# Kernel optimization log

Hardware: AMD Instinct MI355X
Metric: run time of the kernel (lower is better)

## Reference

```python
import jax, jax.numpy as jnp
import numpy as np

B, N, D_POINTS, D_MODEL = 8, 2048, 64, 512


def _linear_params(key, d_in, d_out, bias=True):
    k1, k2 = jax.random.split(key)
    bound = 1.0 / np.sqrt(d_in)
    W = jax.random.uniform(k1, (d_in, d_out), jnp.float32, -bound, bound)
    if not bias:
        return W
    b = jax.random.uniform(k2, (d_out,), jnp.float32, -bound, bound)
    return W, b


def setup_inputs() -> dict:
    key = jax.random.key(0)
    ks = jax.random.split(key, 10)
    xyz = jax.random.normal(ks[0], (B, N, 3), jnp.float32)
    features = jax.random.normal(ks[1], (B, N, D_POINTS), jnp.float32)
    W1, b1 = _linear_params(ks[2], D_POINTS, D_MODEL)      # fc1
    W2, b2 = _linear_params(ks[3], D_MODEL, D_POINTS)      # fc2
    Wd1, bd1 = _linear_params(ks[4], 3, D_MODEL)           # fc_delta[0]
    Wd2, bd2 = _linear_params(ks[5], D_MODEL, D_MODEL)     # fc_delta[2]
    Wq = _linear_params(ks[6], D_MODEL, D_MODEL, bias=False)
    Wk = _linear_params(ks[7], D_MODEL, D_MODEL, bias=False)
    Wv = _linear_params(ks[8], D_MODEL, D_MODEL, bias=False)
    return {"xyz": xyz, "features": features,
            "W1": W1, "b1": b1, "W2": W2, "b2": b2,
            "Wd1": Wd1, "bd1": bd1, "Wd2": Wd2, "bd2": bd2,
            "Wq": Wq, "Wk": Wk, "Wv": Wv, "k": 16}


def _forward(xyz, features, W1, b1, W2, b2, Wd1, bd1, Wd2, bd2, Wq, Wk, Wv, k):
    # square_distance: ||xi - xj||^2, [B, N, N]
    sq = jnp.sum(xyz * xyz, axis=-1)
    dists = sq[:, :, None] + sq[:, None, :] - 2.0 * jnp.einsum('bnd,bmd->bnm', xyz, xyz)
    knn_idx = jnp.argsort(dists, axis=-1)[:, :, :k]              # [B, N, k]
    knn_xyz = jax.vmap(lambda p, i: p[i])(xyz, knn_idx)          # [B, N, k, 3]

    pre = features
    x = features @ W1 + b1                                       # [B, N, d_model]
    q, key, v = x @ Wq, x @ Wk, x @ Wv

    # fc_delta on gathered neighbor coordinates -> [B, N, k, d_model]
    pos_enc = jax.nn.relu(knn_xyz @ Wd1 + bd1) @ Wd2 + bd2

    eps = 1e-06
    knn_d = jnp.take_along_axis(dists, knn_idx, axis=2)          # [B, N, k]
    weights = 1.0 / (knn_d + eps)
    weighted_avg = jnp.sum(pos_enc * weights[..., None], axis=2) / \
        jnp.sum(weights, axis=2, keepdims=True)                  # [B, N, d_model]

    scale = 1.0 / np.sqrt(D_MODEL)
    score = jnp.einsum('bnd,bmd->bnm', q + weighted_avg, key + weighted_avg) * scale
    attn_map = jax.nn.softmax(score, axis=-1)                    # [B, N, N]
    attn = jnp.einsum('bnm,bmd->bnd', attn_map, v + weighted_avg)
    res = attn @ W2 + b2 + pre                                   # [B, N, d_points]
    return res, attn


def reference(xyz, features, W1, b1, W2, b2, Wd1, bd1, Wd2, bd2, Wq, Wk, Wv, k):
    return _forward(xyz, features, W1, b1, W2, b2, Wd1, bd1, Wd2, bd2, Wq, Wk, Wv, k)
```

## Files before the change

kernel.cpp:

```cpp
#include <hip/hip_runtime.h>

#define BB 8
#define NN 2048
#define DP 64
#define DM 512
#define KNNK 16
#define ROWS (BB*NN)

#define SWZ_SK8(t) (((((t)&3) ^ (((t)>>3)&3)))*8)

typedef __attribute__((ext_vector_type(8))) short s16x8;
typedef __attribute__((ext_vector_type(4))) short s16x4;
typedef __attribute__((ext_vector_type(4))) float f32x4;

__device__ __forceinline__ float bf2f(short u){
  union { unsigned int i; float f; } v; v.i = ((unsigned int)(unsigned short)u) << 16; return v.f;
}
__device__ __forceinline__ short f2bf(float f){
  union { float f; unsigned int i; } v; v.f = f;
  unsigned int x = v.i;
  return (short)((x + 0x7fffu + ((x >> 16) & 1u)) >> 16);
}

__device__ __forceinline__ void gload16(const void* g, void* l){
  __builtin_amdgcn_global_load_lds(
      (const __attribute__((address_space(1))) void*)(__UINTPTR_TYPE__)g,
      (__attribute__((address_space(3))) void*)(__UINTPTR_TYPE__)l, 16, 0, 0);
}

__device__ __forceinline__ unsigned wave_min_u32(unsigned v){
  v = min(v, (unsigned)__builtin_amdgcn_update_dpp((int)v, (int)v, 0x111, 0xF, 0xF, false));
  v = min(v, (unsigned)__builtin_amdgcn_update_dpp((int)v, (int)v, 0x112, 0xF, 0xF, false));
  v = min(v, (unsigned)__builtin_amdgcn_update_dpp((int)v, (int)v, 0x114, 0xF, 0xF, false));
  v = min(v, (unsigned)__builtin_amdgcn_update_dpp((int)v, (int)v, 0x118, 0xF, 0xF, false));
  v = min(v, (unsigned)__builtin_amdgcn_update_dpp((int)v, (int)v, 0x142, 0xF, 0xF, false));
  v = min(v, (unsigned)__builtin_amdgcn_update_dpp((int)v, (int)v, 0x143, 0xF, 0xF, false));
  return (unsigned)__builtin_amdgcn_readlane((int)v, 63);
}

__global__ void k_sq(const float* __restrict__ xyz, float* __restrict__ sq){
  int i = blockIdx.x*256 + threadIdx.x;
  if (i < ROWS){
    float x = xyz[3*i], y = xyz[3*i+1], z = xyz[3*i+2];
    sq[i] = x*x + y*y + z*z;
  }
}

__global__ __launch_bounds__(256) void k_knn(const float* __restrict__ xyz, const float* __restrict__ sq,
        int* __restrict__ kidx, float* __restrict__ kw, float* __restrict__ wsum){
  int row = blockIdx.x*4 + (threadIdx.x >> 6);
  int l = threadIdx.x & 63;
  int b = row >> 11; int i = row & (NN-1);
  const float* xb = xyz + (size_t)b*NN*3;
  const float* sqb = sq + (size_t)b*NN;
  float xi0 = xb[3*i], xi1 = xb[3*i+1], xi2 = xb[3*i+2];
  float sqi = sqb[i];
  unsigned key[32];
  unsigned m1 = 0xFFFFFFFFu, m2 = 0xFFFFFFFFu, m3 = 0xFFFFFFFFu;
  #pragma unroll
  for (int e = 0; e < 32; ++e){
    int j = e*64 + l;
    float d = sqi + sqb[j] - 2.0f*(xi0*xb[3*j] + xi1*xb[3*j+1] + xi2*xb[3*j+2]);
    d = fmaxf(d, 0.f);
    union { float f; unsigned u; } cv; cv.f = d;
    unsigned k = (cv.u & 0xFFFFF800u) | (unsigned)j;
    key[e] = k;
    unsigned r1 = max(k, m1);  m1 = min(k, m1);
    unsigned r2 = max(r1, m2); m2 = min(r1, m2);
    m3 = min(r2, m3);
  }
  float wacc = 0.f;
  for (int sel = 0; sel < KNNK; ++sel){
    unsigned g = wave_min_u32(m1);
    unsigned j = g & 2047u;
    union { unsigned u; float f; } dv; dv.u = g & 0xFFFFF800u;
    float wg = 1.0f/(dv.f + 1e-6f);
    wacc += wg;
    if (l == 0){
      kidx[(size_t)row*KNNK + sel] = (int)j;
      kw[(size_t)row*KNNK + sel] = wg;
    }
    bool win = (m1 == g);
    if (win){ m1 = m2; m2 = m3; m3 = 0xFFFFFFFFu; }
    if (__any(win && m1 == 0xFFFFFFFFu)){
      if (win && m1 == 0xFFFFFFFFu){
        unsigned mm = 0xFFFFFFFFu;
        #pragma unroll
        for (int e = 0; e < 32; ++e){
          unsigned k2 = key[e];
          mm = min(mm, (k2 > g) ? k2 : 0xFFFFFFFFu);
        }
        m1 = mm;
      }
    }
  }
  if (l == 0) wsum[row] = wacc;
}

__global__ void k_prep2(const float* __restrict__ Wq, const float* __restrict__ Wk,
                        const float* __restrict__ Wv, const float* __restrict__ Wd2,
                        const float* __restrict__ W1, const float* __restrict__ W2,
                        const float* __restrict__ feat,
                        short* __restrict__ Wqt, short* __restrict__ Wkt,
                        short* __restrict__ Wvt, short* __restrict__ Wd2t,
                        short* __restrict__ W1t, short* __restrict__ W2t,
                        short* __restrict__ featb){
  int idx = blockIdx.x*256 + threadIdx.x;
  if (idx < 4*DM*DM){
    int m = idx >> 18;
    int r = idx & (DM*DM-1);
    int n = r >> 9, k = r & 511;
    const float* W = (m==0)?Wq:(m==1)?Wk:(m==2)?Wv:Wd2;
    short* Wt = (m==0)?Wqt:(m==1)?Wkt:(m==2)?Wvt:Wd2t;
    Wt[r] = f2bf(W[k*DM + n]);
  } else if (idx < 4*DM*DM + DM*DP){
    int r = idx - 4*DM*DM;
    int n = r >> 6, k = r & 63;
    W1t[r] = f2bf(W1[(size_t)k*DM + n]);
  } else if (idx < 4*DM*DM + 2*DM*DP){
    int r = idx - 4*DM*DM - DM*DP;
    int n = r >> 9, k = r & 511;
    W2t[r] = f2bf(W2[(size_t)k*DP + n]);
  } else {
    int r = idx - 4*DM*DM - 2*DM*DP;
    featb[r] = f2bf(feat[r]);
  }
}

__global__ __launch_bounds__(256) void k_g(const float* __restrict__ xyz, const float* __restrict__ Wd1,
                   const float* __restrict__ bd1, const int* __restrict__ kidx,
                   const float* __restrict__ kw, const float* __restrict__ wsum, short* __restrict__ g){
  int bid = blockIdx.x;
  int p = ((bid&7)<<11) + ((bid>>3)<<2) + (threadIdx.x>>6);
  int c8 = (threadIdx.x&63)*8;
  int b = p >> 11;
  const float* xbase = xyz + (size_t)b*NN*3;
  float wd0[8], wd1v[8], wd2v[8], bb[8];
  #pragma unroll
  for (int e=0;e<8;++e){
    wd0[e]  = Wd1[c8+e];
    wd1v[e] = Wd1[DM + c8+e];
    wd2v[e] = Wd1[2*DM + c8+e];
    bb[e]   = bd1[c8+e];
  }
  int jj[KNNK]; float wj[KNNK];
  #pragma unroll
  for (int j = 0; j < KNNK; ++j){
    jj[j] = kidx[(size_t)p*KNNK + j];
    wj[j] = kw[(size_t)p*KNNK + j];
  }
  float acc[8] = {0,0,0,0,0,0,0,0};
  #pragma unroll
  for (int j = 0; j < KNNK; ++j){
    float x0 = xbase[3*jj[j]], x1 = xbase[3*jj[j]+1], x2 = xbase[3*jj[j]+2];
    float w = wj[j];
    #pragma unroll
    for (int e=0;e<8;++e){
      float v = fmaf(x0, wd0[e], fmaf(x1, wd1v[e], fmaf(x2, wd2v[e], bb[e])));
      acc[e] = fmaf(w, fmaxf(v, 0.f), acc[e]);
    }
  }
  float inv = 1.0f/wsum[p];
  s16x8 o;
  #pragma unroll
  for (int e=0;e<8;++e) o[e] = f2bf(acc[e]*inv);
  *(s16x8*)&g[(size_t)p*DM + c8] = o;
}

template<int KD, int MODE>
__global__ __launch_bounds__(256) void k_gemm(const short* __restrict__ A, const short* __restrict__ Bt,
       const float* __restrict__ bias, const short* __restrict__ addb, short* __restrict__ outb){
  __shared__ short As[128*32];
  __shared__ short Bs[128*32];
  int t = threadIdx.x;
  size_t i0 = (size_t)blockIdx.x*128, n0 = (size_t)blockIdx.y*128;
  int w = t >> 6, l = t & 63, la = l & 15, lg = l >> 4;
  int wr = w >> 1, wc = w & 1;
  int rch8 = (lg ^ ((la>>1)&3))*8;
  f32x4 acc[4][4];
  #pragma unroll
  for (int h=0;h<4;++h)
    #pragma unroll
    for (int c=0;c<4;++c) acc[h][c] = (f32x4){0.f,0.f,0.f,0.f};
  int srow = t >> 2; int sk8 = SWZ_SK8(t);
  const short* Ab  = A  + (i0 + srow)*KD + sk8;
  const short* Ab2 = A  + (i0 + 64 + srow)*KD + sk8;
  const short* Bb  = Bt + (n0 + srow)*KD + sk8;
  const short* Bb2 = Bt + (n0 + 64 + srow)*KD + sk8;
  short* Asd  = &As[t*8];      short* Asd2 = &As[2048 + t*8];
  short* Bsd  = &Bs[t*8];      short* Bsd2 = &Bs[2048 + t*8];
  for (int k0 = 0; k0 < KD; k0 += 32){
    gload16(Ab  + k0, Asd);
    gload16(Ab2 + k0, Asd2);
    gload16(Bb  + k0, Bsd);
    gload16(Bb2 + k0, Bsd2);
    __syncthreads();
    s16x8 af[4], bg[4];
    #pragma unroll
    for (int h=0;h<4;++h) af[h] = *(const s16x8*)&As[(wr*64 + h*16 + la)*32 + rch8];
    #pragma unroll
    for (int c=0;c<4;++c) bg[c] = *(const s16x8*)&Bs[(wc*64 + c*16 + la)*32 + rch8];
    #pragma unroll
    for (int h=0;h<4;++h)
      #pragma unroll
      for (int c=0;c<4;++c)
        acc[h][c] = __builtin_amdgcn_mfma_f32_16x16x32_bf16(af[h], bg[c], acc[h][c], 0, 0, 0);
    __syncthreads();
  }
  #pragma unroll
  for (int h=0;h<4;++h){
    #pragma unroll
    for (int c=0;c<4;++c){
      size_t col = n0 + wc*64 + c*16 + la;
      #pragma unroll
      for (int r=0;r<4;++r){
        size_t row = i0 + wr*64 + h*16 + lg*4 + r;
        float v = acc[h][c][r];
        if (MODE == 0) outb[row*DM + col] = f2bf(v + bias[col]);
        else           outb[row*DM + col] = f2bf(v + bf2f(addb[row*DM + col]));
      }
    }
  }
}

__global__ __launch_bounds__(256) void k_vt(const short* __restrict__ ve, short* __restrict__ vt){
  int j0 = blockIdx.x*32, d0 = blockIdx.y*32, b = blockIdx.z;
  __shared__ short tile[32][36];
  int t = threadIdx.x;
  int r = t >> 3, c4 = (t & 7)*4;
  const short* vb = ve + (size_t)b*NN*DM;
  *(s16x4*)&tile[r][c4] = *(const s16x4*)&vb[(size_t)(j0+r)*DM + d0 + c4];
  __syncthreads();
  s16x4 o;
  #pragma unroll
  for (int e=0;e<4;++e) o[e] = tile[c4+e][r];
  short* ob = vt + (size_t)b*DM*NN;
  *(s16x4*)&ob[(size_t)(d0+r)*NN + j0 + c4] = o;
}

__global__ __launch_bounds__(256) void k_sexp(const short* __restrict__ qe, const short* __restrict__ ke,
       short* __restrict__ pbuf, float* __restrict__ lsum_part){
  __shared__ short As[128*32];
  __shared__ short Bs[128*32];
  int bid = blockIdx.x;
  int b = bid & 7;
  int r2 = bid >> 3;
  int ti = r2 & 15, tj = r2 >> 4;
  size_t i0 = (size_t)ti*128;
  size_t j0 = (size_t)tj*128;
  const short* A  = qe + (size_t)b*NN*DM;
  const short* Bt = ke + (size_t)b*NN*DM;
  int t = threadIdx.x;
  int w = t >> 6, l = t & 63, la = l & 15, lg = l >> 4;
  int wr = w >> 1, wc = w & 1;
  int rch8 = (lg ^ ((la>>1)&3))*8;
  f32x4 acc[4][4];
  #pragma unroll
  for (int h=0;h<4;++h)
    #pragma unroll
    for (int c=0;c<4;++c) acc[h][c] = (f32x4){0.f,0.f,0.f,0.f};
  int srow = t >> 2; int sk8 = SWZ_SK8(t);
  const short* Ab  = A  + (i0 + srow)*DM + sk8;
  const short* Ab2 = A  + (i0 + 64 + srow)*DM + sk8;
  const short* Bb  = Bt + (j0 + srow)*DM + sk8;
  const short* Bb2 = Bt + (j0 + 64 + srow)*DM + sk8;
  short* Asd  = &As[t*8];      short* Asd2 = &As[2048 + t*8];
  short* Bsd  = &Bs[t*8];      short* Bsd2 = &Bs[2048 + t*8];
  for (int k0 = 0; k0 < DM; k0 += 32){
    gload16(Ab  + k0, Asd);
    gload16(Ab2 + k0, Asd2);
    gload16(Bb  + k0, Bsd);
    gload16(Bb2 + k0, Bsd2);
    __syncthreads();
    s16x8 af[4], bg[4];
    #pragma unroll
    for (int h=0;h<4;++h) af[h] = *(const s16x8*)&As[(wr*64 + h*16 + la)*32 + rch8];
    #pragma unroll
    for (int c=0;c<4;++c) bg[c] = *(const s16x8*)&Bs[(wc*64 + c*16 + la)*32 + rch8];
    #pragma unroll
    for (int h=0;h<4;++h)
      #pragma unroll
      for (int c=0;c<4;++c)
        acc[h][c] = __builtin_amdgcn_mfma_f32_16x16x32_bf16(af[h], bg[c], acc[h][c], 0, 0, 0);
    __syncthreads();
  }
  const float scale = 0.044194173824159216f;
  short* pb = pbuf + (size_t)b*NN*NN;
  float rsum[4][4];
  #pragma unroll
  for (int h=0;h<4;++h)
    #pragma unroll
    for (int r=0;r<4;++r) rsum[h][r] = 0.f;
  #pragma unroll
  for (int h=0;h<4;++h){
    #pragma unroll
    for (int c=0;c<4;++c){
      size_t col = j0 + wc*64 + c*16 + la;
      #pragma unroll
      for (int r=0;r<4;++r){
        size_t row = i0 + wr*64 + h*16 + lg*4 + r;
        float p = __expf(acc[h][c][r]*scale);
        rsum[h][r] += p;
        pb[row*NN + col] = f2bf(p);
      }
    }
  }
  #pragma unroll
  for (int m = 1; m < 16; m <<= 1){
    #pragma unroll
    for (int h=0;h<4;++h)
      #pragma unroll
      for (int r=0;r<4;++r) rsum[h][r] += __shfl_xor(rsum[h][r], m);
  }
  if (la == 0){
    float* lp = lsum_part + (size_t)(tj*2 + wc)*ROWS + (size_t)b*NN;
    #pragma unroll
    for (int h=0;h<4;++h)
      #pragma unroll
      for (int r=0;r<4;++r)
        lp[i0 + wr*64 + h*16 + lg*4 + r] = rsum[h][r];
  }
}

__global__ void k_lsum(const float* __restrict__ lsum_part, float* __restrict__ linv){
  int g = blockIdx.x*256 + threadIdx.x;
  float s = 0.f;
  #pragma unroll
  for (int i = 0; i < 32; ++i) s += lsum_part[(size_t)i*ROWS + g];
  linv[g] = 1.0f/s;
}

__global__ __launch_bounds__(512) void k_pv(const short* __restrict__ pbuf, const short* __restrict__ vt,
        const float* __restrict__ linv, float* __restrict__ attn, short* __restrict__ attb){
  __shared__ short As[128*32];
  __shared__ short Bs[128*32];
  int bid = blockIdx.x;
  int b = bid & 7;
  int r2 = bid >> 3;
  int ti = r2 & 15, tn = r2 >> 4;
  size_t i0 = (size_t)ti*128;
  size_t n0 = (size_t)tn*128;
  const short* A  = pbuf + (size_t)b*NN*NN;
  const short* Bt = vt + (size_t)b*DM*NN;
  int t = threadIdx.x;
  int w = t >> 6, l = t & 63, la = l & 15, lg = l >> 4;
  int wr = w >> 1, wc = w & 1;
  int rch8 = (lg ^ ((la>>1)&3))*8;
  f32x4 acc[2][4];
  #pragma unroll
  for (int h=0;h<2;++h)
    #pragma unroll
    for (int c=0;c<4;++c) acc[h][c] = (f32x4){0.f,0.f,0.f,0.f};
  int srow = t >> 2; int sk8 = SWZ_SK8(t);
  const short* Ab  = A  + (i0 + srow)*NN + sk8;
  const short* Bb  = Bt + (n0 + srow)*NN + sk8;
  short* Asd  = &As[t*8];
  short* Bsd  = &Bs[t*8];
  for (int k0 = 0; k0 < NN; k0 += 32){
    gload16(Ab + k0, Asd);
    gload16(Bb + k0, Bsd);
    __syncthreads();
    s16x8 af[2], bg[4];
    #pragma unroll
    for (int h=0;h<2;++h) af[h] = *(const s16x8*)&As[(wr*32 + h*16 + la)*32 + rch8];
    #pragma unroll
    for (int c=0;c<4;++c) bg[c] = *(const s16x8*)&Bs[(wc*64 + c*16 + la)*32 + rch8];
    #pragma unroll
    for (int h=0;h<2;++h)
      #pragma unroll
      for (int c=0;c<4;++c)
        acc[h][c] = __builtin_amdgcn_mfma_f32_16x16x32_bf16(af[h], bg[c], acc[h][c], 0, 0, 0);
    __syncthreads();
  }
  #pragma unroll
  for (int h=0;h<2;++h){
    #pragma unroll
    for (int c=0;c<4;++c){
      size_t col = n0 + wc*64 + c*16 + la;
      #pragma unroll
      for (int r=0;r<4;++r){
        size_t row = i0 + wr*32 + h*16 + lg*4 + r;
        float v = acc[h][c][r] * linv[(size_t)b*NN + row];
        size_t off = (size_t)b*NN*DM + row*DM + col;
        attn[off] = v;
        attb[off] = f2bf(v);
      }
    }
  }
}

__global__ __launch_bounds__(256) void k_res(const short* __restrict__ attb, const short* __restrict__ W2t,
       const float* __restrict__ b2, const float* __restrict__ feat, float* __restrict__ res){
  __shared__ short As[64*32];
  __shared__ short Bs[64*32];
  int t = threadIdx.x;
  size_t i0 = (size_t)blockIdx.x*64;
  int w = t >> 6, l = t & 63, la = l & 15, lg = l >> 4;
  int rch8 = (lg ^ ((la>>1)&3))*8;
  f32x4 acc[4];
  #pragma unroll
  for (int c=0;c<4;++c) acc[c] = (f32x4){0.f,0.f,0.f,0.f};
  int srow = t >> 2;
  int sk8 = SWZ_SK8(t);
  for (int k0 = 0; k0 < DM; k0 += 32){
    gload16(attb + (i0 + srow)*DM + k0 + sk8, &As[t*8]);
    gload16(W2t + (size_t)srow*DM + k0 + sk8, &Bs[t*8]);
    __syncthreads();
    s16x8 af, bg[4];
    af = *(const s16x8*)&As[(w*16 + la)*32 + rch8];
    #pragma unroll
    for (int c=0;c<4;++c) bg[c] = *(const s16x8*)&Bs[(c*16 + la)*32 + rch8];
    #pragma unroll
    for (int c=0;c<4;++c)
      acc[c] = __builtin_amdgcn_mfma_f32_16x16x32_bf16(af, bg[c], acc[c], 0, 0, 0);
    __syncthreads();
  }
  #pragma unroll
  for (int c=0;c<4;++c){
    int col = c*16 + la;
    #pragma unroll
    for (int r=0;r<4;++r){
      size_t row = i0 + w*16 + lg*4 + r;
      res[row*DP + col] = acc[c][r] + b2[col] + feat[row*DP + col];
    }
  }
}

extern "C" void kernel_launch(void* const* d_in, const int* in_sizes, int n_in,
                              void* d_out, int out_size, void* d_ws, size_t ws_size,
                              hipStream_t stream){
  const float* xyz  = (const float*)d_in[0];
  const float* feat = (const float*)d_in[1];
  const float* W1   = (const float*)d_in[2];
  const float* b1   = (const float*)d_in[3];
  const float* W2   = (const float*)d_in[4];
  const float* b2   = (const float*)d_in[5];
  const float* Wd1  = (const float*)d_in[6];
  const float* bd1  = (const float*)d_in[7];
  const float* Wd2  = (const float*)d_in[8];
  const float* bd2  = (const float*)d_in[9];
  const float* Wq   = (const float*)d_in[10];
  const float* Wk   = (const float*)d_in[11];
  const float* Wv   = (const float*)d_in[12];

  char* ws = (char*)d_ws;
  float* sq        = (float*)(ws + (0ull<<20));
  int*   kidx      = (int*)  (ws + (1ull<<20));
  float* kw        = (float*)(ws + (2ull<<20));
  float* wsum      = (float*)(ws + (3ull<<20));
  float* lsum_part = (float*)(ws + (1ull<<20));
  float* linv      = (float*)(ws + (3ull<<20));
  short* Wqt   = (short*)(ws + (4ull<<20));
  short* Wkt   = Wqt + (size_t)DM*DM;
  short* Wvt   = Wkt + (size_t)DM*DM;
  short* Wd2t  = Wvt + (size_t)DM*DM;
  short* W1t   = (short*)(ws + (6ull<<20));
  short* W2t   = (short*)(ws + (6ull<<20) + 131072);
  short* featb = (short*)(ws + (7ull<<20));
  short* qe    = (short*)(ws + (9ull<<20));
  short* g     = (short*)(ws + (25ull<<20));
  short* x     = (short*)(ws + (41ull<<20));
  short* wab   = (short*)(ws + (57ull<<20));
  short* ve    = (short*)(ws + (73ull<<20));
  short* pbuf  = (short*)(ws + (89ull<<20));
  short* ke = g; short* vt = x; short* attb = wab;

  float* res  = (float*)d_out;
  float* attn = (float*)d_out + (size_t)ROWS*DP;

  k_sq   <<<ROWS/256, 256, 0, stream>>>(xyz, sq);
  k_knn  <<<ROWS/4, 256, 0, stream>>>(xyz, sq, kidx, kw, wsum);
  k_prep2<<<(4*DM*DM + 2*DM*DP + ROWS*DP)/256, 256, 0, stream>>>(
           Wq, Wk, Wv, Wd2, W1, W2, feat, Wqt, Wkt, Wvt, Wd2t, W1t, W2t, featb);
  k_g    <<<ROWS/4, 256, 0, stream>>>(xyz, Wd1, bd1, kidx, kw, wsum, g);
  k_gemm<DP,0>  <<<dim3(ROWS/128, DM/128), 256, 0, stream>>>(featb, W1t, b1, nullptr, x);
  k_gemm<DM,0>  <<<dim3(ROWS/128, DM/128), 256, 0, stream>>>(g, Wd2t, bd2, nullptr, wab);
  k_gemm<DM,1>  <<<dim3(ROWS/128, DM/128), 256, 0, stream>>>(x, Wqt, nullptr, wab, qe);
  k_gemm<DM,1>  <<<dim3(ROWS/128, DM/128), 256, 0, stream>>>(x, Wkt, nullptr, wab, ke);
  k_gemm<DM,1>  <<<dim3(ROWS/128, DM/128), 256, 0, stream>>>(x, Wvt, nullptr, wab, ve);
  k_vt   <<<dim3(NN/32, DM/32, BB), 256, 0, stream>>>(ve, vt);
  k_sexp <<<2048, 256, 0, stream>>>(qe, ke, pbuf, lsum_part);
  k_lsum <<<ROWS/256, 256, 0, stream>>>(lsum_part, linv);
  k_pv   <<<512, 512, 0, stream>>>(pbuf, vt, linv, attn, attb);
  k_res  <<<ROWS/64, 256, 0, stream>>>(attb, W2t, b2, feat, res);
}
```

Baseline: 257.7 us.

## Fuse Q/K/V projections into one launch, remap attention block order, drop bf16 attn copy

The three Q, K and V projection GEMMs become one kernel with a 12-column grid that picks its output buffer per block, relying on Wq/Wk/Wv being stored contiguously. The k_sexp and k_pv block-index mappings are reordered so blocks running at the same time share batch and row tiles, aiming for better L2 reuse. k_pv no longer writes a separate bf16 copy of attn; k_res instead reads the fp32 attn output and converts it to bf16 while staging into LDS. This cuts launches and global writes, but k_res now reads twice the bytes through non-async loads.

After: 258.9 us. No clear change (+0.4%).

```diff
diff --git a/kernel.cpp b/kernel.cpp
--- a/kernel.cpp
+++ b/kernel.cpp
@@ -223,6 +223,63 @@
   }
 }
 
+__global__ __launch_bounds__(256) void k_gemm3(const short* __restrict__ A, const short* __restrict__ Bt,
+       const short* __restrict__ addb, short* __restrict__ q, short* __restrict__ k, short* __restrict__ v){
+  __shared__ short As[128*32];
+  __shared__ short Bs[128*32];
+  int t = threadIdx.x;
+  int by = blockIdx.y;
+  short* outb = (by < 4) ? q : (by < 8) ? k : v;
+  size_t i0 = (size_t)blockIdx.x*128;
+  size_t n0 = (size_t)by*128;
+  size_t c0 = (size_t)(by & 3)*128;
+  int w = t >> 6, l = t & 63, la = l & 15, lg = l >> 4;
+  int wr = w >> 1, wc = w & 1;
+  int rch8 = (lg ^ ((la>>1)&3))*8;
+  f32x4 acc[4][4];
+  #pragma unroll
+  for (int h=0;h<4;++h)
+    #pragma unroll
+    for (int c=0;c<4;++c) acc[h][c] = (f32x4){0.f,0.f,0.f,0.f};
+  int srow = t >> 2; int sk8 = SWZ_SK8(t);
+  const short* Ab  = A  + (i0 + srow)*DM + sk8;
+  const short* Ab2 = A  + (i0 + 64 + srow)*DM + sk8;
+  const short* Bb  = Bt + (n0 + srow)*DM + sk8;
+  const short* Bb2 = Bt + (n0 + 64 + srow)*DM + sk8;
+  short* Asd  = &As[t*8];      short* Asd2 = &As[2048 + t*8];
+  short* Bsd  = &Bs[t*8];      short* Bsd2 = &Bs[2048 + t*8];
+  for (int k0 = 0; k0 < DM; k0 += 32){
+    gload16(Ab  + k0, Asd);
+    gload16(Ab2 + k0, Asd2);
+    gload16(Bb  + k0, Bsd);
+    gload16(Bb2 + k0, Bsd2);
+    __syncthreads();
+    s16x8 af[4], bg[4];
+    #pragma unroll
+    for (int h=0;h<4;++h) af[h] = *(const s16x8*)&As[(wr*64 + h*16 + la)*32 + rch8];
+    #pragma unroll
+    for (int c=0;c<4;++c) bg[c] = *(const s16x8*)&Bs[(wc*64 + c*16 + la)*32 + rch8];
+    #pragma unroll
+    for (int h=0;h<4;++h)
+      #pragma unroll
+      for (int c=0;c<4;++c)
+        acc[h][c] = __builtin_amdgcn_mfma_f32_16x16x32_bf16(af[h], bg[c], acc[h][c], 0, 0, 0);
+    __syncthreads();
+  }
+  #pragma unroll
+  for (int h=0;h<4;++h){
+    #pragma unroll
+    for (int c=0;c<4;++c){
+      size_t col = c0 + wc*64 + c*16 + la;
+      #pragma unroll
+      for (int r=0;r<4;++r){
+        size_t row = i0 + wr*64 + h*16 + lg*4 + r;
+        outb[row*DM + col] = f2bf(acc[h][c][r] + bf2f(addb[row*DM + col]));
+      }
+    }
+  }
+}
+
 __global__ __launch_bounds__(256) void k_vt(const short* __restrict__ ve, short* __restrict__ vt){
   int j0 = blockIdx.x*32, d0 = blockIdx.y*32, b = blockIdx.z;
   __shared__ short tile[32][36];
@@ -243,9 +300,12 @@
   __shared__ short As[128*32];
   __shared__ short Bs[128*32];
   int bid = blockIdx.x;
-  int b = bid & 7;
-  int r2 = bid >> 3;
-  int ti = r2 & 15, tj = r2 >> 4;
+  int xg = bid & 7;
+  int y  = bid >> 3;
+  int tj = y & 15;
+  int g  = (y >> 4)*8 + xg;
+  int b  = g >> 4;
+  int ti = g & 15;
   size_t i0 = (size_t)ti*128;
   size_t j0 = (size_t)tj*128;
   const short* A  = qe + (size_t)b*NN*DM;
@@ -331,13 +391,16 @@
 }
 
 __global__ __launch_bounds__(512) void k_pv(const short* __restrict__ pbuf, const short* __restrict__ vt,
-        const float* __restrict__ linv, float* __restrict__ attn, short* __restrict__ attb){
+        const float* __restrict__ linv, float* __restrict__ attn){
   __shared__ short As[128*32];
   __shared__ short Bs[128*32];
   int bid = blockIdx.x;
-  int b = bid & 7;
-  int r2 = bid >> 3;
-  int ti = r2 & 15, tn = r2 >> 4;
+  int xg = bid & 7;
+  int y  = bid >> 3;
+  int tn = y & 3;
+  int g  = (y >> 2)*8 + xg;
+  int b  = g >> 4;
+  int ti = g & 15;
   size_t i0 = (size_t)ti*128;
   size_t n0 = (size_t)tn*128;
   const short* A  = pbuf + (size_t)b*NN*NN;
@@ -380,16 +443,13 @@
       #pragma unroll
       for (int r=0;r<4;++r){
         size_t row = i0 + wr*32 + h*16 + lg*4 + r;
-        float v = acc[h][c][r] * linv[(size_t)b*NN + row];
-        size_t off = (size_t)b*NN*DM + row*DM + col;
-        attn[off] = v;
-        attb[off] = f2bf(v);
+        attn[(size_t)b*NN*DM + row*DM + col] = acc[h][c][r] * linv[(size_t)b*NN + row];
       }
     }
   }
 }
 
-__global__ __launch_bounds__(256) void k_res(const short* __restrict__ attb, const short* __restrict__ W2t,
+__global__ __launch_bounds__(256) void k_res(const float* __restrict__ attn, const short* __restrict__ W2t,
        const float* __restrict__ b2, const float* __restrict__ feat, float* __restrict__ res){
   __shared__ short As[64*32];
   __shared__ short Bs[64*32];
@@ -401,9 +461,17 @@
   #pragma unroll
   for (int c=0;c<4;++c) acc[c] = (f32x4){0.f,0.f,0.f,0.f};
   int srow = t >> 2;
+  int ch = t & 3;
+  int dsw8 = (ch ^ ((srow>>1)&3))*8;
   int sk8 = SWZ_SK8(t);
+  const float* Arow = attn + (i0 + srow)*DM + ch*8;
   for (int k0 = 0; k0 < DM; k0 += 32){
-    gload16(attb + (i0 + srow)*DM + k0 + sk8, &As[t*8]);
+    f32x4 a0 = *(const f32x4*)&Arow[k0];
+    f32x4 a1 = *(const f32x4*)&Arow[k0 + 4];
+    s16x8 ab;
+    #pragma unroll
+    for (int e=0;e<4;++e){ ab[e] = f2bf(a0[e]); ab[4+e] = f2bf(a1[e]); }
+    *(s16x8*)&As[srow*32 + dsw8] = ab;
     gload16(W2t + (size_t)srow*DM + k0 + sk8, &Bs[t*8]);
     __syncthreads();
     s16x8 af, bg[4];
@@ -463,7 +531,7 @@
   short* wab   = (short*)(ws + (57ull<<20));
   short* ve    = (short*)(ws + (73ull<<20));
   short* pbuf  = (short*)(ws + (89ull<<20));
-  short* ke = g; short* vt = x; short* attb = wab;
+  short* ke = g; short* vt = x;
 
   float* res  = (float*)d_out;
   float* attn = (float*)d_out + (size_t)ROWS*DP;
@@ -475,12 +543,10 @@
   k_g    <<<ROWS/4, 256, 0, stream>>>(xyz, Wd1, bd1, kidx, kw, wsum, g);
   k_gemm<DP,0>  <<<dim3(ROWS/128, DM/128), 256, 0, stream>>>(featb, W1t, b1, nullptr, x);
   k_gemm<DM,0>  <<<dim3(ROWS/128, DM/128), 256, 0, stream>>>(g, Wd2t, bd2, nullptr, wab);
-  k_gemm<DM,1>  <<<dim3(ROWS/128, DM/128), 256, 0, stream>>>(x, Wqt, nullptr, wab, qe);
-  k_gemm<DM,1>  <<<dim3(ROWS/128, DM/128), 256, 0, stream>>>(x, Wkt, nullptr, wab, ke);
-  k_gemm<DM,1>  <<<dim3(ROWS/128, DM/128), 256, 0, stream>>>(x, Wvt, nullptr, wab, ve);
+  k_gemm3       <<<dim3(ROWS/128, 12), 256, 0, stream>>>(x, Wqt, wab, qe, ke, ve);
   k_vt   <<<dim3(NN/32, DM/32, BB), 256, 0, stream>>>(ve, vt);
   k_sexp <<<2048, 256, 0, stream>>>(qe, ke, pbuf, lsum_part);
   k_lsum <<<ROWS/256, 256, 0, stream>>>(lsum_part, linv);
-  k_pv   <<<512, 512, 0, stream>>>(pbuf, vt, linv, attn, attb);
-  k_res  <<<ROWS/64, 256, 0, stream>>>(attb, W2t, b2, feat, res);
-}
+  k_pv   <<<512, 512, 0, stream>>>(pbuf, vt, linv, attn);
+  k_res  <<<ROWS/64, 256, 0, stream>>>(attn, W2t, b2, feat, res);
+}
```
